# Kernel tuning notes

Hardware: AMD Instinct MI355X
Metric: run time of the kernel (lower is better)

The kernel has to match this reference:

```python
import jax, jax.numpy as jnp
import numpy as np

B, F_DIM, FH, FW = 2, 2048, 64, 128
C, H, W = 19, 512, 1024


def resize_bilinear_ac(x, h, w):
    # align_corners=True bilinear resize of (B, C, H, W) -> (B, C, h, w)
    Bx, Cx, Hx, Wx = x.shape
    ys = jnp.linspace(0.0, Hx - 1.0, h)
    xs = jnp.linspace(0.0, Wx - 1.0, w)
    y0 = jnp.floor(ys).astype(jnp.int32)
    y1 = jnp.minimum(y0 + 1, Hx - 1)
    wy = (ys - y0).astype(x.dtype)
    x0 = jnp.floor(xs).astype(jnp.int32)
    x1 = jnp.minimum(x0 + 1, Wx - 1)
    wx = (xs - x0).astype(x.dtype)
    r = x[:, :, y0, :] * (1 - wy)[None, None, :, None] + x[:, :, y1, :] * wy[None, None, :, None]
    return r[:, :, :, x0] * (1 - wx) + r[:, :, :, x1] * wx


def setup_inputs() -> dict:
    key = jax.random.key(0)
    k1, k2, k3, k4 = jax.random.split(key, 4)
    return {
        "source_feat": jax.random.normal(k1, (B, F_DIM, FH, FW), dtype=jnp.float32),
        "source_softmax": jax.random.uniform(k2, (B, C, H, W), dtype=jnp.float32),
        "target_feat": jax.random.normal(k3, (B, F_DIM, FH, FW), dtype=jnp.float32),
        "target_softmax": jax.random.uniform(k4, (B, C, H, W), dtype=jnp.float32),
        "norm_order": 2,
    }


def _process(feat, softmax):
    # feat: (B, F, h, w) -> (B*h*w, F); labels from bilinear-downsampled softmax argmax
    h, w = feat.shape[2], feat.shape[3]
    f2 = feat.transpose(0, 2, 3, 1).reshape(-1, feat.shape[1])
    sm_dws = resize_bilinear_ac(softmax, h, w)
    labels = jnp.argmax(sm_dws, axis=1).reshape(-1)
    return f2, labels


def _forward(source_feat, source_softmax, target_feat, target_softmax, p):
    num_class = source_softmax.shape[1]
    fdim = source_feat.shape[1]
    sf, sl = _process(source_feat, source_softmax)
    tf, tl = _process(target_feat, target_softmax)

    # mixed centroids: per-class mean over concatenated source+target pixels
    sum_s = jax.ops.segment_sum(sf, sl, num_segments=num_class)
    cnt_s = jax.ops.segment_sum(jnp.ones(sf.shape[0], sf.dtype), sl, num_segments=num_class)
    sum_t = jax.ops.segment_sum(tf, tl, num_segments=num_class)
    cnt_t = jax.ops.segment_sum(jnp.ones(tf.shape[0], tf.dtype), tl, num_segments=num_class)
    cnt = cnt_s + cnt_t
    seen = cnt > 0
    centroids = (sum_s + sum_t) / jnp.maximum(cnt, 1.0)[:, None]  # (C, F)

    inv_p = 1.0 / p

    def f_dist(f2, lab, cnt_d):
        # torch: sum_i norm(centroid_i - feat_i, p) / (n_i * F) over classes with n_i>0, / count
        dp = jnp.sum(jnp.abs(f2 - centroids[lab]) ** p, axis=1)  # (N,)
        ssq = jax.ops.segment_sum(dp, lab, num_segments=num_class)  # (C,)
        valid = cnt_d > 0
        ssq_safe = jnp.where(valid, ssq, 1.0)
        per = ssq_safe ** inv_p / (jnp.maximum(cnt_d, 1.0) * fdim)
        return jnp.sum(jnp.where(valid, per, 0.0)) / jnp.sum(valid).astype(f2.dtype)

    f_dist_source = f_dist(sf, sl, cnt_s)
    f_dist_target = f_dist(tf, tl, cnt_t)

    # intra-domain centroid-to-centroid distance over seen classes
    n_seen = jnp.sum(seen).astype(centroids.dtype)
    diffp = jnp.sum(jnp.abs(centroids[:, None, :] - centroids[None, :, :]) ** p, axis=-1)  # (C, C)
    pair_mask = seen[:, None] & seen[None, :] & (~jnp.eye(num_class, dtype=bool))
    row = jnp.sum(jnp.where(pair_mask, diffp, 0.0), axis=1)
    row_safe = jnp.where(seen, row, 1.0)
    per_i = row_safe ** inv_p / ((n_seen - 1.0) * fdim)
    c_dist = jnp.sum(jnp.where(seen, per_i, 0.0)) / n_seen

    return jnp.stack([c_dist, f_dist_source, f_dist_target])


def reference(source_feat, source_softmax, target_feat, target_softmax, norm_order):
    return _forward(source_feat, source_softmax, target_feat, target_softmax, norm_order)
```

## Files before the change

kernel.cpp:

```cpp
#include <hip/hip_runtime.h>
#include <hip/hip_bf16.h>

#define BB 2
#define FDIM 2048
#define FH 64
#define FW 128
#define NPIX (FH*FW)
#define NC 19
#define SH 512
#define SW 1024

#define KS 4
#define PXS (NPIX/KS)
#define NSTAGE (PXS/256)

#define OFF_PSQ   0
#define OFF_CNT   1216
#define OFF_SUM   1408
#define ZERO_BYTES 312704
#define OFF_LAB   312704
#define OFF_CENT  345472
#define OFF_DOTS  501120
#define OFF_ROW   501348

typedef __attribute__((ext_vector_type(8))) short short8v;
typedef __attribute__((ext_vector_type(4))) float f32x4;

__device__ inline short f32_to_bf16_bits(float x) {
  __hip_bfloat16 h = __float2bfloat16(x);
  return *reinterpret_cast<short*>(&h);
}
__device__ inline float bf16_bits_to_f32(short s) {
  unsigned u = ((unsigned)s & 0xFFFFu) << 16;
  return __uint_as_float(u);
}

__global__ __launch_bounds__(256) void labels_kernel(
    const float* __restrict__ sm_s, const float* __restrict__ sm_t,
    unsigned char* __restrict__ labels, unsigned int* __restrict__ cnt) {
  __shared__ unsigned int lcnt[NC];
  int tid = threadIdx.x;
  if (tid < NC) lcnt[tid] = 0u;
  __syncthreads();

  int g = blockIdx.x * 256 + tid;
  int pixid = g >> 2;
  int sub = g & 3;
  int dom = pixid >> 14;
  int rem = pixid & 16383;
  int b   = rem >> 13;
  int pix = rem & (NPIX - 1);
  int oy  = pix >> 7;
  int ox  = pix & (FW - 1);

  const float* sm = dom ? sm_t : sm_s;

  const float step_y = 511.0f / 63.0f;
  const float step_x = 1023.0f / 127.0f;
  float fy = __fmul_rn((float)oy, step_y);
  float fx = __fmul_rn((float)ox, step_x);
  int y0 = (int)floorf(fy); int y1 = min(y0 + 1, SH - 1);
  int x0 = (int)floorf(fx); int x1 = min(x0 + 1, SW - 1);
  float wy = __fsub_rn(fy, (float)y0);
  float wx = __fsub_rn(fx, (float)x0);
  float omwy = __fsub_rn(1.0f, wy);
  float omwx = __fsub_rn(1.0f, wx);

  const float* base = sm + (size_t)b * (NC * SH * SW);
  float best = -1.0f; int bestc = 127;
  for (int c = sub; c < NC; c += 4) {
    const float* p = base + (size_t)c * (SH * SW);
    float v00 = p[y0 * SW + x0];
    float v01 = p[y0 * SW + x1];
    float v10 = p[y1 * SW + x0];
    float v11 = p[y1 * SW + x1];
    float r0  = __fadd_rn(__fmul_rn(v00, omwy), __fmul_rn(v10, wy));
    float r1  = __fadd_rn(__fmul_rn(v01, omwy), __fmul_rn(v11, wy));
    float val = __fadd_rn(__fmul_rn(r0, omwx), __fmul_rn(r1, wx));
    if (val > best) { best = val; bestc = c; }
  }
#pragma unroll
  for (int off = 1; off <= 2; off <<= 1) {
    float ov = __shfl_xor(best, off, 64);
    int   oc = __shfl_xor(bestc, off, 64);
    if (ov > best || (ov == best && oc < bestc)) { best = ov; bestc = oc; }
  }
  if (sub == 0) {
    labels[pixid] = (unsigned char)bestc;
    atomicAdd(&lcnt[bestc], 1u);
  }
  __syncthreads();
  if (tid < NC) atomicAdd(&cnt[dom * NC + tid], lcnt[tid]);
}

__global__ __launch_bounds__(256, 6) void segsum_kernel(
    const float* __restrict__ feat_s, const float* __restrict__ feat_t,
    const unsigned char* __restrict__ labels,
    float* __restrict__ sum, float* __restrict__ psq) {
  __shared__ unsigned short Abuf[2][16][256];
  __shared__ unsigned char  Lbuf[2][256];

  int tid = threadIdx.x;
  int wv = tid >> 6, l = tid & 63;
  int m16 = l & 15, grp = l >> 4;

  int low = blockIdx.x & 255;
  int hi  = blockIdx.x >> 8;
  int d = low >> 7, strip = low & 127;
  int b = hi & 1, ks = hi >> 1;

  const float* feat = d ? feat_t : feat_s;
  const float* fbase = feat + ((size_t)(b * FDIM + strip * 16)) * NPIX + ks * PXS;
  const unsigned char* labp = labels + (d * 2 + b) * NPIX + ks * PXS;

  float4 ld[4];
#pragma unroll
  for (int r = 0; r < 4; ++r)
    ld[r] = *(const float4*)(fbase + (size_t)(r * 4 + wv) * NPIX + l * 4);
  uint2 lwstage = make_uint2(0u, 0u);
  if (tid < 32) lwstage = *(const uint2*)(labp + tid * 8);

#pragma unroll
  for (int r = 0; r < 4; ++r) {
    int row = r * 4 + wv;
    unsigned u0 = ((unsigned)(unsigned short)f32_to_bf16_bits(ld[r].x)) |
                  (((unsigned)(unsigned short)f32_to_bf16_bits(ld[r].y)) << 16);
    unsigned u1 = ((unsigned)(unsigned short)f32_to_bf16_bits(ld[r].z)) |
                  (((unsigned)(unsigned short)f32_to_bf16_bits(ld[r].w)) << 16);
    int wbyte = (l * 8) ^ ((row & 7) << 4);
    *(uint2*)((char*)&Abuf[0][row][0] + wbyte) = make_uint2(u0, u1);
  }
  if (tid < 32) *(uint2*)&Lbuf[0][tid * 8] = lwstage;
  __syncthreads();

  f32x4 accS0 = {0.f,0.f,0.f,0.f}, accS1 = {0.f,0.f,0.f,0.f};
  f32x4 accQ0 = {0.f,0.f,0.f,0.f}, accQ1 = {0.f,0.f,0.f,0.f};

  for (int s = 0; s < NSTAGE; ++s) {
    int cur = s & 1;
    if (s < NSTAGE - 1) {
#pragma unroll
      for (int r = 0; r < 4; ++r)
        ld[r] = *(const float4*)(fbase + (size_t)(r * 4 + wv) * NPIX +
                                 (s + 1) * 256 + l * 4);
      if (tid < 32) lwstage = *(const uint2*)(labp + (s + 1) * 256 + tid * 8);
    }
#pragma unroll
    for (int t = 0; t < 2; ++t) {
      int kt = wv * 2 + t;
      int k0 = kt * 32 + grp * 8;
      int rbyte = (k0 * 2) ^ ((m16 & 7) << 4);
      short8v a = *(const short8v*)((const char*)&Abuf[cur][m16][0] + rbyte);
      short8v a2;
#pragma unroll
      for (int j = 0; j < 8; ++j) {
        float x = bf16_bits_to_f32(a[j]);
        a2[j] = f32_to_bf16_bits(x * x);
      }
      uint2 lw = *(const uint2*)&Lbuf[cur][k0];
      short8v b0, b1;
#pragma unroll
      for (int j = 0; j < 8; ++j) {
        unsigned lab = ((j < 4 ? lw.x : lw.y) >> ((j & 3) * 8)) & 0xFFu;
        b0[j] = (lab == (unsigned)m16)        ? (short)0x3F80 : (short)0;
        b1[j] = (lab == (unsigned)(m16 + 16)) ? (short)0x3F80 : (short)0;
      }
      accS0 = __builtin_amdgcn_mfma_f32_16x16x32_bf16(a,  b0, accS0, 0, 0, 0);
      accS1 = __builtin_amdgcn_mfma_f32_16x16x32_bf16(a,  b1, accS1, 0, 0, 0);
      accQ0 = __builtin_amdgcn_mfma_f32_16x16x32_bf16(a2, b0, accQ0, 0, 0, 0);
      accQ1 = __builtin_amdgcn_mfma_f32_16x16x32_bf16(a2, b1, accQ1, 0, 0, 0);
    }
    __syncthreads();
    if (s < NSTAGE - 1) {
#pragma unroll
      for (int r = 0; r < 4; ++r) {
        int row = r * 4 + wv;
        unsigned u0 = ((unsigned)(unsigned short)f32_to_bf16_bits(ld[r].x)) |
                      (((unsigned)(unsigned short)f32_to_bf16_bits(ld[r].y)) << 16);
        unsigned u1 = ((unsigned)(unsigned short)f32_to_bf16_bits(ld[r].z)) |
                      (((unsigned)(unsigned short)f32_to_bf16_bits(ld[r].w)) << 16);
        int wbyte = (l * 8) ^ ((row & 7) << 4);
        *(uint2*)((char*)&Abuf[cur ^ 1][row][0] + wbyte) = make_uint2(u0, u1);
      }
      if (tid < 32) *(uint2*)&Lbuf[cur ^ 1][tid * 8] = lwstage;
      __syncthreads();
    }
  }

  float* Sred = (float*)&Abuf[0][0][0];
  float* Qred = Sred + 4 * 19 * 16;

  int c0 = l & 15, frb = (l >> 4) * 4;
  *(f32x4*)&Sred[(wv * 19 + c0) * 16 + frb] = accS0;
  if (c0 < 3) *(f32x4*)&Sred[(wv * 19 + 16 + c0) * 16 + frb] = accS1;

  float q0 = accQ0[0] + accQ0[1] + accQ0[2] + accQ0[3];
  float q1 = accQ1[0] + accQ1[1] + accQ1[2] + accQ1[3];
  q0 += __shfl_xor(q0, 16, 64); q0 += __shfl_xor(q0, 32, 64);
  q1 += __shfl_xor(q1, 16, 64); q1 += __shfl_xor(q1, 32, 64);
  if (l < 16) Qred[wv * 19 + l] = q0;
  if (l < 3)  Qred[wv * 19 + 16 + l] = q1;
  __syncthreads();

  for (int t = tid; t < NC * 16; t += 256) {
    int c = t >> 4, fr = t & 15;
    float sv = Sred[(0 * 19 + c) * 16 + fr] + Sred[(1 * 19 + c) * 16 + fr] +
               Sred[(2 * 19 + c) * 16 + fr] + Sred[(3 * 19 + c) * 16 + fr];
    unsafeAtomicAdd(&sum[((size_t)d * NC + c) * FDIM + strip * 16 + fr], sv);
  }
  if (tid < NC) {
    float qv = Qred[tid] + Qred[19 + tid] + Qred[38 + tid] + Qred[57 + tid];
    unsafeAtomicAdd(&psq[(blockIdx.x & 7) * (2 * NC) + d * NC + tid], qv);
  }
}

__device__ inline float block_reduce(float v, float* red, int tid) {
  red[tid] = v; __syncthreads();
  for (int s = 128; s > 0; s >>= 1) {
    if (tid < s) red[tid] += red[tid + s];
    __syncthreads();
  }
  float r = red[0];
  __syncthreads();
  return r;
}

__global__ __launch_bounds__(256) void centroid_kernel(
    const float* __restrict__ sum, const unsigned int* __restrict__ cnt,
    float* __restrict__ cent, float* __restrict__ dots) {
  __shared__ float red[256];
  int c = blockIdx.x;
  int tid = threadIdx.x;
  float cs = (float)cnt[c];
  float ct = (float)cnt[NC + c];
  float denom = fmaxf(cs + ct, 1.0f);
  float ds = 0.f, dt = 0.f, cc = 0.f;
  for (int f = tid; f < FDIM; f += 256) {
    float ssv = sum[(size_t)c * FDIM + f];
    float stv = sum[(size_t)(NC + c) * FDIM + f];
    float cf = (ssv + stv) / denom;
    cent[(size_t)c * FDIM + f] = cf;
    ds += cf * ssv; dt += cf * stv; cc += cf * cf;
  }
  float rds = block_reduce(ds, red, tid);
  float rdt = block_reduce(dt, red, tid);
  float rcc = block_reduce(cc, red, tid);
  if (tid == 0) {
    dots[c] = rds;
    dots[NC + c] = rdt;
    dots[2 * NC + c] = rcc;
  }
}

__global__ __launch_bounds__(256) void pair_kernel(
    const float* __restrict__ cent, const unsigned int* __restrict__ cnt,
    float* __restrict__ row) {
  __shared__ float red[256];
  int i = blockIdx.x;
  int tid = threadIdx.x;
  bool seen_i = (cnt[i] + cnt[NC + i]) > 0u;
  float acc = 0.f;
  if (seen_i) {
    for (int j = 0; j < NC; ++j) {
      if (j == i) continue;
      if ((cnt[j] + cnt[NC + j]) == 0u) continue;
      for (int f = tid; f < FDIM; f += 256) {
        float dd = cent[(size_t)i * FDIM + f] - cent[(size_t)j * FDIM + f];
        acc += dd * dd;
      }
    }
  }
  float r = block_reduce(acc, red, tid);
  if (tid == 0) row[i] = r;
}

__global__ void final_kernel(
    const unsigned int* __restrict__ cnt, const float* __restrict__ psq,
    const float* __restrict__ dots, const float* __restrict__ row,
    float* __restrict__ out) {
  int l = threadIdx.x;
  const float fdim = (float)FDIM;
  bool isC = l < NC;
  int c = isC ? l : 0;

  float cs = 0.f, ct = 0.f, qs = 0.f, qt = 0.f;
  float d_s = 0.f, d_t = 0.f, cc = 0.f, rw = 0.f;
  if (isC) {
    cs = (float)cnt[c]; ct = (float)cnt[NC + c];
#pragma unroll
    for (int x = 0; x < 8; ++x) {
      qs += psq[x * (2 * NC) + c];
      qt += psq[x * (2 * NC) + NC + c];
    }
    d_s = dots[c]; d_t = dots[NC + c]; cc = dots[2 * NC + c];
    rw = row[c];
  }
  bool seen = isC && (cs + ct > 0.f);
  float nseenf = (float)__popcll(__ballot(seen));
  float nvs    = (float)__popcll(__ballot(isC && cs > 0.f));
  float nvt    = (float)__popcll(__ballot(isC && ct > 0.f));

  float fs = 0.f, ft = 0.f, cd = 0.f;
  if (isC && cs > 0.f) {
    float ssq = fmaxf(qs - 2.0f * d_s + cs * cc, 0.f);
    fs = sqrtf(ssq) / (cs * fdim);
  }
  if (isC && ct > 0.f) {
    float ssq = fmaxf(qt - 2.0f * d_t + ct * cc, 0.f);
    ft = sqrtf(ssq) / (ct * fdim);
  }
  if (seen) cd = sqrtf(rw) / ((nseenf - 1.0f) * fdim);

#pragma unroll
  for (int off = 32; off > 0; off >>= 1) {
    fs += __shfl_down(fs, off, 64);
    ft += __shfl_down(ft, off, 64);
    cd += __shfl_down(cd, off, 64);
  }
  if (l == 0) {
    out[0] = cd / nseenf;
    out[1] = fs / nvs;
    out[2] = ft / nvt;
  }
}

extern "C" void kernel_launch(void* const* d_in, const int* in_sizes, int n_in,
                              void* d_out, int out_size, void* d_ws, size_t ws_size,
                              hipStream_t stream) {
  const float* sfeat = (const float*)d_in[0];
  const float* ssm   = (const float*)d_in[1];
  const float* tfeat = (const float*)d_in[2];
  const float* tsm   = (const float*)d_in[3];
  float* out = (float*)d_out;

  char* ws = (char*)d_ws;
  float*         psq    = (float*)(ws + OFF_PSQ);
  unsigned int*  cnt    = (unsigned int*)(ws + OFF_CNT);
  float*         sum    = (float*)(ws + OFF_SUM);
  unsigned char* labels = (unsigned char*)(ws + OFF_LAB);
  float*         cent   = (float*)(ws + OFF_CENT);
  float*         dots   = (float*)(ws + OFF_DOTS);
  float*         row    = (float*)(ws + OFF_ROW);

  hipMemsetAsync(ws, 0, ZERO_BYTES, stream);

  labels_kernel  <<<512,  256, 0, stream>>>(ssm, tsm, labels, cnt);
  segsum_kernel  <<<2048, 256, 0, stream>>>(sfeat, tfeat, labels, sum, psq);
  centroid_kernel<<<NC,   256, 0, stream>>>(sum, cnt, cent, dots);
  pair_kernel    <<<NC,   256, 0, stream>>>(cent, cnt, row);
  final_kernel   <<<1,    64,  0, stream>>>(cnt, psq, dots, row, out);
}
```

Before: 120.5 us.

## Give each wave a private pixel chunk and LDS buffer, dropping block barriers

The segment-sum kernel now gives each of the four waves its own contiguous 512-pixel range and a private double-buffered LDS tile. This removes the two block-wide __syncthreads per stage and the shared label staging; labels are read straight from global memory. Global feature loads become shorter row segments of 256 bytes instead of 1 KB, which may hurt coalescing. The occupancy hint in launch bounds drops from 6 to 4 blocks per SIMD, giving the compiler more register room.

Measured after the change: 111.6 us. 7.4% less time.

```diff
diff --git a/kernel.cpp b/kernel.cpp
--- a/kernel.cpp
+++ b/kernel.cpp
@@ -12,7 +12,6 @@
 
 #define KS 4
 #define PXS (NPIX/KS)
-#define NSTAGE (PXS/256)
 
 #define OFF_PSQ   0
 #define OFF_CNT   1216
@@ -93,16 +92,17 @@
   if (tid < NC) atomicAdd(&cnt[dom * NC + tid], lcnt[tid]);
 }
 
-__global__ __launch_bounds__(256, 6) void segsum_kernel(
+__global__ __launch_bounds__(256, 4) void segsum_kernel(
     const float* __restrict__ feat_s, const float* __restrict__ feat_t,
     const unsigned char* __restrict__ labels,
     float* __restrict__ sum, float* __restrict__ psq) {
-  __shared__ unsigned short Abuf[2][16][256];
-  __shared__ unsigned char  Lbuf[2][256];
+  __shared__ unsigned short Abuf[4][2][16][64];
 
   int tid = threadIdx.x;
   int wv = tid >> 6, l = tid & 63;
   int m16 = l & 15, grp = l >> 4;
+  int lrow = l >> 4;
+  int lpx  = (l & 15) * 4;
 
   int low = blockIdx.x & 255;
   int hi  = blockIdx.x >> 8;
@@ -110,54 +110,51 @@
   int b = hi & 1, ks = hi >> 1;
 
   const float* feat = d ? feat_t : feat_s;
-  const float* fbase = feat + ((size_t)(b * FDIM + strip * 16)) * NPIX + ks * PXS;
-  const unsigned char* labp = labels + (d * 2 + b) * NPIX + ks * PXS;
-
-  float4 ld[4];
-#pragma unroll
-  for (int r = 0; r < 4; ++r)
-    ld[r] = *(const float4*)(fbase + (size_t)(r * 4 + wv) * NPIX + l * 4);
-  uint2 lwstage = make_uint2(0u, 0u);
-  if (tid < 32) lwstage = *(const uint2*)(labp + tid * 8);
-
-#pragma unroll
-  for (int r = 0; r < 4; ++r) {
-    int row = r * 4 + wv;
-    unsigned u0 = ((unsigned)(unsigned short)f32_to_bf16_bits(ld[r].x)) |
-                  (((unsigned)(unsigned short)f32_to_bf16_bits(ld[r].y)) << 16);
-    unsigned u1 = ((unsigned)(unsigned short)f32_to_bf16_bits(ld[r].z)) |
-                  (((unsigned)(unsigned short)f32_to_bf16_bits(ld[r].w)) << 16);
-    int wbyte = (l * 8) ^ ((row & 7) << 4);
-    *(uint2*)((char*)&Abuf[0][row][0] + wbyte) = make_uint2(u0, u1);
-  }
-  if (tid < 32) *(uint2*)&Lbuf[0][tid * 8] = lwstage;
-  __syncthreads();
+  int px0 = ks * PXS + wv * 512;
+  const float* fbase = feat + ((size_t)(b * FDIM + strip * 16)) * NPIX + px0;
+  const unsigned char* labp = labels + (d * 2 + b) * NPIX + px0;
+
+  unsigned short (*mybuf)[16][64] = Abuf[wv];
 
   f32x4 accS0 = {0.f,0.f,0.f,0.f}, accS1 = {0.f,0.f,0.f,0.f};
   f32x4 accQ0 = {0.f,0.f,0.f,0.f}, accQ1 = {0.f,0.f,0.f,0.f};
 
-  for (int s = 0; s < NSTAGE; ++s) {
-    int cur = s & 1;
-    if (s < NSTAGE - 1) {
-#pragma unroll
-      for (int r = 0; r < 4; ++r)
-        ld[r] = *(const float4*)(fbase + (size_t)(r * 4 + wv) * NPIX +
-                                 (s + 1) * 256 + l * 4);
-      if (tid < 32) lwstage = *(const uint2*)(labp + (s + 1) * 256 + tid * 8);
-    }
+  float4 ld[4];
+
+#define LOADW(W)                                                              \
+  _Pragma("unroll") for (int r = 0; r < 4; ++r)                               \
+    ld[r] = *(const float4*)(fbase + (size_t)(r * 4 + lrow) * NPIX +          \
+                             (W) * 64 + lpx);
+
+#define WRITEW(CUR)                                                           \
+  _Pragma("unroll") for (int r = 0; r < 4; ++r) {                             \
+    int row = r * 4 + lrow;                                                   \
+    unsigned u0 = ((unsigned)(unsigned short)f32_to_bf16_bits(ld[r].x)) |     \
+                  (((unsigned)(unsigned short)f32_to_bf16_bits(ld[r].y)) << 16);\
+    unsigned u1 = ((unsigned)(unsigned short)f32_to_bf16_bits(ld[r].z)) |     \
+                  (((unsigned)(unsigned short)f32_to_bf16_bits(ld[r].w)) << 16);\
+    int wbyte = (row * 128 + lpx * 2) ^ ((row & 7) << 4);                     \
+    *(uint2*)((char*)&mybuf[CUR][0][0] + wbyte) = make_uint2(u0, u1);         \
+  }
+
+  LOADW(0);
+  WRITEW(0);
+
+#pragma unroll 2
+  for (int w = 0; w < 8; ++w) {
+    int cur = w & 1;
+    if (w < 7) { LOADW(w + 1); }
 #pragma unroll
     for (int t = 0; t < 2; ++t) {
-      int kt = wv * 2 + t;
-      int k0 = kt * 32 + grp * 8;
-      int rbyte = (k0 * 2) ^ ((m16 & 7) << 4);
-      short8v a = *(const short8v*)((const char*)&Abuf[cur][m16][0] + rbyte);
+      int rbyte = (m16 * 128 + t * 64 + grp * 16) ^ ((m16 & 7) << 4);
+      short8v a = *(const short8v*)((const char*)&mybuf[cur][0][0] + rbyte);
       short8v a2;
 #pragma unroll
       for (int j = 0; j < 8; ++j) {
         float x = bf16_bits_to_f32(a[j]);
         a2[j] = f32_to_bf16_bits(x * x);
       }
-      uint2 lw = *(const uint2*)&Lbuf[cur][k0];
+      uint2 lw = *(const uint2*)(labp + w * 64 + t * 32 + grp * 8);
       short8v b0, b1;
 #pragma unroll
       for (int j = 0; j < 8; ++j) {
@@ -170,24 +167,13 @@
       accQ0 = __builtin_amdgcn_mfma_f32_16x16x32_bf16(a2, b0, accQ0, 0, 0, 0);
       accQ1 = __builtin_amdgcn_mfma_f32_16x16x32_bf16(a2, b1, accQ1, 0, 0, 0);
     }
-    __syncthreads();
-    if (s < NSTAGE - 1) {
-#pragma unroll
-      for (int r = 0; r < 4; ++r) {
-        int row = r * 4 + wv;
-        unsigned u0 = ((unsigned)(unsigned short)f32_to_bf16_bits(ld[r].x)) |
-                      (((unsigned)(unsigned short)f32_to_bf16_bits(ld[r].y)) << 16);
-        unsigned u1 = ((unsigned)(unsigned short)f32_to_bf16_bits(ld[r].z)) |
-                      (((unsigned)(unsigned short)f32_to_bf16_bits(ld[r].w)) << 16);
-        int wbyte = (l * 8) ^ ((row & 7) << 4);
-        *(uint2*)((char*)&Abuf[cur ^ 1][row][0] + wbyte) = make_uint2(u0, u1);
-      }
-      if (tid < 32) *(uint2*)&Lbuf[cur ^ 1][tid * 8] = lwstage;
-      __syncthreads();
-    }
-  }
-
-  float* Sred = (float*)&Abuf[0][0][0];
+    if (w < 7) { WRITEW(cur ^ 1); }
+  }
+#undef LOADW
+#undef WRITEW
+
+  __syncthreads();
+  float* Sred = (float*)&Abuf[0][0][0][0];
   float* Qred = Sred + 4 * 19 * 16;
 
   int c0 = l & 15, frb = (l >> 4) * 4;
```
